# Optimization experiments

Hardware: AMD Instinct MI355X
Metric: run time of the kernel (lower is better)

The kernel has to match this reference:

```python
import jax, jax.numpy as jnp
import numpy as np

N_NODES = 100000
N_EDGES = 1600000
NODE_D = 64
EDGE_D = 48
U_D = 32
N_GRAPHS = 64
HIDDEN = 128
OUT_D = 64
IN_D = NODE_D + EDGE_D + U_D  # 144


def setup_inputs() -> dict:
    key = jax.random.key(0)
    ks = jax.random.split(key, 10)
    x = jax.random.normal(ks[0], (N_NODES, NODE_D), dtype=jnp.float32)
    edge_index = jax.random.randint(ks[1], (2, N_EDGES), 0, N_NODES, dtype=jnp.int64)
    edge_attr = jax.random.normal(ks[2], (N_EDGES, EDGE_D), dtype=jnp.float32)
    u = jax.random.normal(ks[3], (N_GRAPHS, U_D), dtype=jnp.float32)
    batch = jnp.sort(jax.random.randint(ks[4], (N_NODES,), 0, N_GRAPHS, dtype=jnp.int64))
    # FCNN params: Linear(144,128) -> relu -> Linear(128,128) -> relu -> Linear(128,64)
    W1 = jax.random.normal(ks[5], (IN_D, HIDDEN), dtype=jnp.float32) / np.sqrt(IN_D)
    b1 = jnp.zeros((HIDDEN,), dtype=jnp.float32)
    W2 = jax.random.normal(ks[6], (HIDDEN, HIDDEN), dtype=jnp.float32) / np.sqrt(HIDDEN)
    b2 = jnp.zeros((HIDDEN,), dtype=jnp.float32)
    W3 = jax.random.normal(ks[7], (HIDDEN, OUT_D), dtype=jnp.float32) / np.sqrt(HIDDEN)
    b3 = jnp.zeros((OUT_D,), dtype=jnp.float32)
    return {"x": x, "edge_index": edge_index, "edge_attr": edge_attr, "u": u,
            "batch": batch, "W1": W1, "b1": b1, "W2": W2, "b2": b2, "W3": W3, "b3": b3}


def reference(x, edge_index, edge_attr, u, batch, W1, b1, W2, b2, W3, b3):
    n = x.shape[0]
    seg = edge_index[0]  # source node per edge
    # scatter_mean(edge_attr, edge_index[0], dim=0) -> [N, edge_d]
    sums = jax.ops.segment_sum(edge_attr, seg, num_segments=n)
    cnt = jax.ops.segment_sum(jnp.ones((edge_attr.shape[0],), edge_attr.dtype), seg, num_segments=n)
    v_e = sums / jnp.maximum(cnt, 1.0)[:, None]  # mean, 0 for empty segments
    comb = jnp.concatenate([x, v_e, u[batch]], axis=1)  # [N, 144]
    h = jax.nn.relu(comb @ W1 + b1)
    h = jax.nn.relu(h @ W2 + b2)
    return h @ W3 + b3
```

## Files before the change

kernel.cpp:

```cpp
#include <hip/hip_runtime.h>
#include <hip/hip_bf16.h>

#define NN 100000
#define NE 1600000
#define NODE_D 64
#define EDGE_D 48
#define U_D 32
#define IN_D 144
#define HID 128
#define OUT_D 64
#define BM 64
#define S0 152
#define S1 136
#define SCAN_BS 1024
#define SCAN_NB ((NN + SCAN_BS - 1) / SCAN_BS)

typedef __attribute__((ext_vector_type(8))) short bf16x8;
typedef __attribute__((ext_vector_type(4))) float f32x4;

__device__ __forceinline__ short f2bs(float f) {
  union { __hip_bfloat16 h; short s; } v;
  v.h = __float2bfloat16(f);
  return v.s;
}

__device__ __forceinline__ void st4(unsigned short* p, float4 v) {
  unsigned a = (unsigned)(unsigned short)f2bs(v.x) | ((unsigned)(unsigned short)f2bs(v.y) << 16);
  unsigned b = (unsigned)(unsigned short)f2bs(v.z) | ((unsigned)(unsigned short)f2bs(v.w) << 16);
  *reinterpret_cast<uint2*>(p) = make_uint2(a, b);
}

__global__ __launch_bounds__(256) void hist_kernel(const int* __restrict__ src,
                                                   int* __restrict__ hist) {
  int e = blockIdx.x * 256 + threadIdx.x;
  if (e >= NE) return;
  atomicAdd(&hist[src[e]], 1);
}

__global__ __launch_bounds__(256) void bsum_kernel(const int* __restrict__ hist,
                                                   int* __restrict__ bsum) {
  const int b = blockIdx.x, tid = threadIdx.x;
  const int base = b * SCAN_BS + tid * 4;
  int4 v = make_int4(0, 0, 0, 0);
  if (base + 3 < NN) v = *reinterpret_cast<const int4*>(&hist[base]);
  else {
    int t[4] = {0, 0, 0, 0};
    for (int k = 0; k < 4; ++k) if (base + k < NN) t[k] = hist[base + k];
    v = make_int4(t[0], t[1], t[2], t[3]);
  }
  int s = v.x + v.y + v.z + v.w;
  for (int d = 32; d; d >>= 1) s += __shfl_down(s, d, 64);
  __shared__ int ws[4];
  if ((tid & 63) == 0) ws[tid >> 6] = s;
  __syncthreads();
  if (tid == 0) bsum[b] = ws[0] + ws[1] + ws[2] + ws[3];
}

__global__ __launch_bounds__(128) void bscan_kernel(const int* __restrict__ bsum,
                                                    int* __restrict__ bpre) {
  const int t = threadIdx.x;
  const int lane = t & 63, wave = t >> 6;
  int v = (t < SCAN_NB) ? bsum[t] : 0;
  int incl = v;
  for (int d = 1; d < 64; d <<= 1) {
    int q = __shfl_up(incl, d, 64);
    if (lane >= d) incl += q;
  }
  __shared__ int wtot[2];
  if (lane == 63) wtot[wave] = incl;
  __syncthreads();
  int add = (wave == 1) ? wtot[0] : 0;
  if (t < SCAN_NB) bpre[t] = incl - v + add;
}

__global__ __launch_bounds__(256) void offsets_kernel(const int* __restrict__ hist,
                                                      const int* __restrict__ bpre,
                                                      int* __restrict__ offsets,
                                                      int* __restrict__ cursor) {
  const int b = blockIdx.x, tid = threadIdx.x;
  const int base = b * SCAN_BS + tid * 4;
  const int lane = tid & 63, wave = tid >> 6;
  int4 v = make_int4(0, 0, 0, 0);
  if (base + 3 < NN) v = *reinterpret_cast<const int4*>(&hist[base]);
  else {
    int t[4] = {0, 0, 0, 0};
    for (int k = 0; k < 4; ++k) if (base + k < NN) t[k] = hist[base + k];
    v = make_int4(t[0], t[1], t[2], t[3]);
  }
  const int tsum = v.x + v.y + v.z + v.w;
  int incl = tsum;
  for (int d = 1; d < 64; d <<= 1) {
    int q = __shfl_up(incl, d, 64);
    if (lane >= d) incl += q;
  }
  __shared__ int ws[4];
  __shared__ int wpre[4];
  if (lane == 63) ws[wave] = incl;
  __syncthreads();
  if (tid == 0) {
    int r = 0;
    for (int w = 0; w < 4; ++w) { wpre[w] = r; r += ws[w]; }
  }
  __syncthreads();
  int run = bpre[b] + wpre[wave] + incl - tsum;
  int vals[4] = {v.x, v.y, v.z, v.w};
  for (int k = 0; k < 4; ++k) {
    int i = base + k;
    if (i < NN) { offsets[i] = run; cursor[i] = run; run += vals[k]; }
  }
}

__global__ __launch_bounds__(256) void permute_kernel(const int* __restrict__ src,
                                                      int* __restrict__ cursor,
                                                      int* __restrict__ perm) {
  int e = blockIdx.x * 256 + threadIdx.x;
  if (e >= NE) return;
  int s = src[e];
  int pos = atomicAdd(&cursor[s], 1);
  perm[pos] = e;
}

__global__ __launch_bounds__(256) void gather_mean_kernel(
    const float* __restrict__ ea, const int* __restrict__ perm,
    const int* __restrict__ hist, const int* __restrict__ offsets,
    unsigned short* __restrict__ mean) {
  const int node = (blockIdx.x * 256 + threadIdx.x) >> 6;
  const int lane = threadIdx.x & 63;
  if (node >= NN) return;
  const int g = lane >> 4;
  const int c = lane & 15;
  const int deg = hist[node];
  const int off = offsets[node];

  float4 acc = make_float4(0.f, 0.f, 0.f, 0.f);
  if (c < 12) {
    const float* bc = ea + (size_t)c * 4;
    int j = g;
    for (; j + 4 < deg; j += 8) {
      int e0 = perm[off + j];
      int e1 = perm[off + j + 4];
      float4 v0 = *reinterpret_cast<const float4*>(bc + (size_t)e0 * EDGE_D);
      float4 v1 = *reinterpret_cast<const float4*>(bc + (size_t)e1 * EDGE_D);
      acc.x += v0.x + v1.x;
      acc.y += v0.y + v1.y;
      acc.z += v0.z + v1.z;
      acc.w += v0.w + v1.w;
    }
    if (j < deg) {
      int e0 = perm[off + j];
      float4 v0 = *reinterpret_cast<const float4*>(bc + (size_t)e0 * EDGE_D);
      acc.x += v0.x; acc.y += v0.y; acc.z += v0.z; acc.w += v0.w;
    }
  }
#pragma unroll
  for (int d = 32; d >= 16; d >>= 1) {
    acc.x += __shfl_xor(acc.x, d, 64);
    acc.y += __shfl_xor(acc.y, d, 64);
    acc.z += __shfl_xor(acc.z, d, 64);
    acc.w += __shfl_xor(acc.w, d, 64);
  }
  if (lane < 12) {
    float inv = (deg > 0) ? 1.0f / (float)deg : 0.0f;
    st4(&mean[(size_t)node * EDGE_D + lane * 4],
        make_float4(acc.x * inv, acc.y * inv, acc.z * inv, acc.w * inv));
  }
}

__global__ __launch_bounds__(256) void mlp_kernel(
    const float* __restrict__ x, const unsigned short* __restrict__ mean,
    const float* __restrict__ u, const int* __restrict__ batch,
    const float* __restrict__ W1, const float* __restrict__ b1,
    const float* __restrict__ W2, const float* __restrict__ b2,
    const float* __restrict__ W3, const float* __restrict__ b3,
    float* __restrict__ out) {
  __shared__ unsigned short act0[BM][S0];
  __shared__ unsigned short act1[BM][S1];

  const int tid = threadIdx.x;
  const int lane = tid & 63;
  const int wid = tid >> 6;
  const int lr = lane & 15;
  const int lg = lane >> 4;
  const int node0 = blockIdx.x * BM;

  const bf16x8 az = {0, 0, 0, 0, 0, 0, 0, 0};

  for (int i = tid; i < BM * (NODE_D / 4); i += 256) {
    int r = i >> 4, q = i & 15;
    int node = node0 + r;
    float4 v = make_float4(0.f, 0.f, 0.f, 0.f);
    if (node < NN) v = reinterpret_cast<const float4*>(x)[(size_t)node * 16 + q];
    st4(&act0[r][q * 4], v);
  }
  for (int i = tid; i < BM * (EDGE_D / 4); i += 256) {
    int r = i / 12, q = i - r * 12;
    int node = node0 + r;
    uint2 v = make_uint2(0, 0);
    if (node < NN) v = *reinterpret_cast<const uint2*>(&mean[(size_t)node * EDGE_D + q * 4]);
    *reinterpret_cast<uint2*>(&act0[r][NODE_D + q * 4]) = v;
  }
  for (int i = tid; i < BM * (U_D / 4); i += 256) {
    int r = i >> 3, q = i & 7;
    int node = node0 + r;
    float4 v = make_float4(0.f, 0.f, 0.f, 0.f);
    if (node < NN) {
      int b = batch[node];
      v = reinterpret_cast<const float4*>(u)[(size_t)b * 8 + q];
    }
    st4(&act0[r][NODE_D + EDGE_D + q * 4], v);
  }
  __syncthreads();

  {
    const int n0 = wid * 32;
    bf16x8 wf[5][2];
#pragma unroll
    for (int t = 0; t < 5; ++t) {
#pragma unroll
      for (int nf = 0; nf < 2; ++nf) {
        const int kb = t * 32 + lg * 8;
        const int n = n0 + nf * 16 + lr;
        bf16x8 r = az;
#pragma unroll
        for (int j = 0; j < 8; ++j) {
          int k = kb + j;
          if (k < IN_D) r[j] = f2bs(W1[(size_t)k * HID + n]);
        }
        wf[t][nf] = r;
      }
    }
    float bias0 = b1[n0 + lr], bias1 = b1[n0 + 16 + lr];
    f32x4 acc[4][2];
#pragma unroll
    for (int mf = 0; mf < 4; ++mf) {
      acc[mf][0] = (f32x4){bias0, bias0, bias0, bias0};
      acc[mf][1] = (f32x4){bias1, bias1, bias1, bias1};
    }
#pragma unroll
    for (int t = 0; t < 5; ++t) {
#pragma unroll
      for (int mf = 0; mf < 4; ++mf) {
        bf16x8 a;
        if (t < 4) {
          a = *reinterpret_cast<const bf16x8*>(&act0[mf * 16 + lr][t * 32 + lg * 8]);
        } else {
          a = az;
          if (lg < 2)
            a = *reinterpret_cast<const bf16x8*>(&act0[mf * 16 + lr][128 + lg * 8]);
        }
        acc[mf][0] = __builtin_amdgcn_mfma_f32_16x16x32_bf16(a, wf[t][0], acc[mf][0], 0, 0, 0);
        acc[mf][1] = __builtin_amdgcn_mfma_f32_16x16x32_bf16(a, wf[t][1], acc[mf][1], 0, 0, 0);
      }
    }
#pragma unroll
    for (int mf = 0; mf < 4; ++mf)
#pragma unroll
      for (int nf = 0; nf < 2; ++nf)
#pragma unroll
        for (int r = 0; r < 4; ++r)
          act1[mf * 16 + lg * 4 + r][n0 + nf * 16 + lr] =
              (unsigned short)f2bs(fmaxf(acc[mf][nf][r], 0.f));
  }
  __syncthreads();

  {
    const int n0 = wid * 32;
    bf16x8 wf[4][2];
#pragma unroll
    for (int t = 0; t < 4; ++t) {
#pragma unroll
      for (int nf = 0; nf < 2; ++nf) {
        const int kb = t * 32 + lg * 8;
        const int n = n0 + nf * 16 + lr;
        bf16x8 r;
#pragma unroll
        for (int j = 0; j < 8; ++j) r[j] = f2bs(W2[(size_t)(kb + j) * HID + n]);
        wf[t][nf] = r;
      }
    }
    float bias0 = b2[n0 + lr], bias1 = b2[n0 + 16 + lr];
    f32x4 acc[4][2];
#pragma unroll
    for (int mf = 0; mf < 4; ++mf) {
      acc[mf][0] = (f32x4){bias0, bias0, bias0, bias0};
      acc[mf][1] = (f32x4){bias1, bias1, bias1, bias1};
    }
#pragma unroll
    for (int t = 0; t < 4; ++t) {
#pragma unroll
      for (int mf = 0; mf < 4; ++mf) {
        bf16x8 a = *reinterpret_cast<const bf16x8*>(&act1[mf * 16 + lr][t * 32 + lg * 8]);
        acc[mf][0] = __builtin_amdgcn_mfma_f32_16x16x32_bf16(a, wf[t][0], acc[mf][0], 0, 0, 0);
        acc[mf][1] = __builtin_amdgcn_mfma_f32_16x16x32_bf16(a, wf[t][1], acc[mf][1], 0, 0, 0);
      }
    }
    __syncthreads();
#pragma unroll
    for (int mf = 0; mf < 4; ++mf)
#pragma unroll
      for (int nf = 0; nf < 2; ++nf)
#pragma unroll
        for (int r = 0; r < 4; ++r)
          act0[mf * 16 + lg * 4 + r][n0 + nf * 16 + lr] =
              (unsigned short)f2bs(fmaxf(acc[mf][nf][r], 0.f));
  }
  __syncthreads();

  {
    const int n0 = wid * 16;
    bf16x8 wf[4];
#pragma unroll
    for (int t = 0; t < 4; ++t) {
      const int kb = t * 32 + lg * 8;
      const int n = n0 + lr;
      bf16x8 r;
#pragma unroll
      for (int j = 0; j < 8; ++j) r[j] = f2bs(W3[(size_t)(kb + j) * OUT_D + n]);
      wf[t] = r;
    }
    float bias = b3[n0 + lr];
    f32x4 acc[4];
#pragma unroll
    for (int mf = 0; mf < 4; ++mf) acc[mf] = (f32x4){bias, bias, bias, bias};
#pragma unroll
    for (int t = 0; t < 4; ++t) {
#pragma unroll
      for (int mf = 0; mf < 4; ++mf) {
        bf16x8 a = *reinterpret_cast<const bf16x8*>(&act0[mf * 16 + lr][t * 32 + lg * 8]);
        acc[mf] = __builtin_amdgcn_mfma_f32_16x16x32_bf16(a, wf[t], acc[mf], 0, 0, 0);
      }
    }
#pragma unroll
    for (int mf = 0; mf < 4; ++mf)
#pragma unroll
      for (int r = 0; r < 4; ++r) {
        int node = node0 + mf * 16 + lg * 4 + r;
        if (node < NN) out[(size_t)node * OUT_D + n0 + lr] = acc[mf][r];
      }
  }
}

extern "C" void kernel_launch(void* const* d_in, const int* in_sizes, int n_in,
                              void* d_out, int out_size, void* d_ws, size_t ws_size,
                              hipStream_t stream) {
  const float* x   = (const float*)d_in[0];
  const int* ei    = (const int*)d_in[1];
  const float* ea  = (const float*)d_in[2];
  const float* u   = (const float*)d_in[3];
  const int* batch = (const int*)d_in[4];
  const float* W1  = (const float*)d_in[5];
  const float* b1  = (const float*)d_in[6];
  const float* W2  = (const float*)d_in[7];
  const float* b2  = (const float*)d_in[8];
  const float* W3  = (const float*)d_in[9];
  const float* b3  = (const float*)d_in[10];
  float* out = (float*)d_out;

  unsigned short* mean = (unsigned short*)d_ws;
  int* hist    = (int*)(mean + (size_t)NN * EDGE_D);
  int* offsets = hist + NN;
  int* cursor  = offsets + NN;
  int* perm    = cursor + NN;
  int* bsum    = perm + NE;
  int* bpre    = bsum + SCAN_NB;

  hipMemsetAsync(hist, 0, NN * sizeof(int), stream);

  hist_kernel<<<(NE + 255) / 256, 256, 0, stream>>>(ei, hist);
  bsum_kernel<<<SCAN_NB, 256, 0, stream>>>(hist, bsum);
  bscan_kernel<<<1, 128, 0, stream>>>(bsum, bpre);
  offsets_kernel<<<SCAN_NB, 256, 0, stream>>>(hist, bpre, offsets, cursor);
  permute_kernel<<<(NE + 255) / 256, 256, 0, stream>>>(ei, cursor, perm);
  gather_mean_kernel<<<(NN * 64 + 255) / 256, 256, 0, stream>>>(ea, perm, hist, offsets, mean);
  mlp_kernel<<<(NN + BM - 1) / BM, 256, 0, stream>>>(x, mean, u, batch,
                                                     W1, b1, W2, b2, W3, b3, out);
}
```

Measured before the change: 339.7 us.

## Fuse edge-mean gather into MLP kernel and prepack bf16 weights

Moves the per-node edge-attribute mean gather into the MLP kernel, writing the means straight into shared memory instead of round-tripping a bf16 mean buffer through global memory. Weights are converted once to bf16 in a transposed layout by a setup kernel that also zeroes the histogram, replacing hipMemsetAsync and the per-block strided scalar weight conversion. The histogram and permute kernels now handle two edges per thread with int2 loads, and permute uses nontemporal stores. Running the gather inside the MLP blocks lowers gather parallelism per node (16 lanes per node, 4 nodes sequentially per group), which may hurt latency hiding.

```diff
diff --git a/kernel.cpp b/kernel.cpp
--- a/kernel.cpp
+++ b/kernel.cpp
@@ -14,6 +14,11 @@
 #define S1 136
 #define SCAN_BS 1024
 #define SCAN_NB ((NN + SCAN_BS - 1) / SCAN_BS)
+#define W1K 160
+#define NW1 (HID * W1K)
+#define NW2 (HID * HID)
+#define NW3 (OUT_D * HID)
+#define NWTOT (NW1 + NW2 + NW3)
 
 typedef __attribute__((ext_vector_type(8))) short bf16x8;
 typedef __attribute__((ext_vector_type(4))) float f32x4;
@@ -30,11 +35,45 @@
   *reinterpret_cast<uint2*>(p) = make_uint2(a, b);
 }
 
+__global__ __launch_bounds__(256) void setup_kernel(
+    int* __restrict__ hist,
+    const float* __restrict__ W1, const float* __restrict__ W2,
+    const float* __restrict__ W3, unsigned short* __restrict__ Wp) {
+  const int b = blockIdx.x, tid = threadIdx.x;
+  if (b < SCAN_NB) {
+    int base = b * SCAN_BS + tid * 4;
+    if (base + 3 < NN) {
+      *reinterpret_cast<int4*>(&hist[base]) = make_int4(0, 0, 0, 0);
+    } else {
+      for (int k = 0; k < 4; ++k)
+        if (base + k < NN) hist[base + k] = 0;
+    }
+    return;
+  }
+  int gid = (b - SCAN_NB) * 256 + tid;
+  if (gid >= NWTOT) return;
+  float v;
+  if (gid < NW1) {
+    int n = gid / W1K, k = gid - n * W1K;
+    v = (k < IN_D) ? W1[(size_t)k * HID + n] : 0.f;
+  } else if (gid < NW1 + NW2) {
+    int i2 = gid - NW1;
+    int n = i2 >> 7, k = i2 & 127;
+    v = W2[(size_t)k * HID + n];
+  } else {
+    int i3 = gid - NW1 - NW2;
+    int n = i3 >> 7, k = i3 & 127;
+    v = W3[(size_t)k * OUT_D + n];
+  }
+  Wp[gid] = (unsigned short)f2bs(v);
+}
+
 __global__ __launch_bounds__(256) void hist_kernel(const int* __restrict__ src,
                                                    int* __restrict__ hist) {
-  int e = blockIdx.x * 256 + threadIdx.x;
-  if (e >= NE) return;
-  atomicAdd(&hist[src[e]], 1);
+  int i = blockIdx.x * 256 + threadIdx.x;
+  int2 s = *reinterpret_cast<const int2*>(&src[i * 2]);
+  atomicAdd(&hist[s.x], 1);
+  atomicAdd(&hist[s.y], 1);
 }
 
 __global__ __launch_bounds__(256) void bsum_kernel(const int* __restrict__ hist,
@@ -113,66 +152,22 @@
 __global__ __launch_bounds__(256) void permute_kernel(const int* __restrict__ src,
                                                       int* __restrict__ cursor,
                                                       int* __restrict__ perm) {
-  int e = blockIdx.x * 256 + threadIdx.x;
-  if (e >= NE) return;
-  int s = src[e];
-  int pos = atomicAdd(&cursor[s], 1);
-  perm[pos] = e;
-}
-
-__global__ __launch_bounds__(256) void gather_mean_kernel(
-    const float* __restrict__ ea, const int* __restrict__ perm,
-    const int* __restrict__ hist, const int* __restrict__ offsets,
-    unsigned short* __restrict__ mean) {
-  const int node = (blockIdx.x * 256 + threadIdx.x) >> 6;
-  const int lane = threadIdx.x & 63;
-  if (node >= NN) return;
-  const int g = lane >> 4;
-  const int c = lane & 15;
-  const int deg = hist[node];
-  const int off = offsets[node];
-
-  float4 acc = make_float4(0.f, 0.f, 0.f, 0.f);
-  if (c < 12) {
-    const float* bc = ea + (size_t)c * 4;
-    int j = g;
-    for (; j + 4 < deg; j += 8) {
-      int e0 = perm[off + j];
-      int e1 = perm[off + j + 4];
-      float4 v0 = *reinterpret_cast<const float4*>(bc + (size_t)e0 * EDGE_D);
-      float4 v1 = *reinterpret_cast<const float4*>(bc + (size_t)e1 * EDGE_D);
-      acc.x += v0.x + v1.x;
-      acc.y += v0.y + v1.y;
-      acc.z += v0.z + v1.z;
-      acc.w += v0.w + v1.w;
-    }
-    if (j < deg) {
-      int e0 = perm[off + j];
-      float4 v0 = *reinterpret_cast<const float4*>(bc + (size_t)e0 * EDGE_D);
-      acc.x += v0.x; acc.y += v0.y; acc.z += v0.z; acc.w += v0.w;
-    }
-  }
-#pragma unroll
-  for (int d = 32; d >= 16; d >>= 1) {
-    acc.x += __shfl_xor(acc.x, d, 64);
-    acc.y += __shfl_xor(acc.y, d, 64);
-    acc.z += __shfl_xor(acc.z, d, 64);
-    acc.w += __shfl_xor(acc.w, d, 64);
-  }
-  if (lane < 12) {
-    float inv = (deg > 0) ? 1.0f / (float)deg : 0.0f;
-    st4(&mean[(size_t)node * EDGE_D + lane * 4],
-        make_float4(acc.x * inv, acc.y * inv, acc.z * inv, acc.w * inv));
-  }
-}
-
-__global__ __launch_bounds__(256) void mlp_kernel(
-    const float* __restrict__ x, const unsigned short* __restrict__ mean,
+  int i = blockIdx.x * 256 + threadIdx.x;
+  int2 s = *reinterpret_cast<const int2*>(&src[i * 2]);
+  int e0 = i * 2, e1 = i * 2 + 1;
+  int p0 = atomicAdd(&cursor[s.x], 1);
+  __builtin_nontemporal_store(e0, &perm[p0]);
+  int p1 = atomicAdd(&cursor[s.y], 1);
+  __builtin_nontemporal_store(e1, &perm[p1]);
+}
+
+__global__ __launch_bounds__(256) void fused_kernel(
+    const float* __restrict__ x, const float* __restrict__ ea,
     const float* __restrict__ u, const int* __restrict__ batch,
-    const float* __restrict__ W1, const float* __restrict__ b1,
-    const float* __restrict__ W2, const float* __restrict__ b2,
-    const float* __restrict__ W3, const float* __restrict__ b3,
-    float* __restrict__ out) {
+    const int* __restrict__ perm, const int* __restrict__ hist,
+    const int* __restrict__ offsets, const unsigned short* __restrict__ Wp,
+    const float* __restrict__ b1, const float* __restrict__ b2,
+    const float* __restrict__ b3, float* __restrict__ out) {
   __shared__ unsigned short act0[BM][S0];
   __shared__ unsigned short act1[BM][S1];
 
@@ -183,7 +178,58 @@
   const int lg = lane >> 4;
   const int node0 = blockIdx.x * BM;
 
+  const unsigned short* Wp1 = Wp;
+  const unsigned short* Wp2 = Wp + NW1;
+  const unsigned short* Wp3 = Wp + NW1 + NW2;
+
   const bf16x8 az = {0, 0, 0, 0, 0, 0, 0, 0};
+
+  {
+    const int g = tid >> 4;
+    const int c = tid & 15;
+    const int gb = (g & 3) * 16;
+    for (int i = 0; i < 4; ++i) {
+      const int nl = g * 4 + i;
+      const int node = node0 + nl;
+      int deg = 0, off = 0;
+      if (node < NN) { deg = hist[node]; off = offsets[node]; }
+      float4 acc = make_float4(0.f, 0.f, 0.f, 0.f);
+      for (int base = 0; base < deg; base += 16) {
+        int rem = deg - base;
+        int m = rem < 16 ? rem : 16;
+        int pv = 0;
+        if (c < m) pv = perm[off + base + c];
+        int jj = 0;
+        for (; jj + 3 < m; jj += 4) {
+          int e0 = __shfl(pv, gb + jj, 64);
+          int e1 = __shfl(pv, gb + jj + 1, 64);
+          int e2 = __shfl(pv, gb + jj + 2, 64);
+          int e3 = __shfl(pv, gb + jj + 3, 64);
+          if (c < 12) {
+            float4 v0 = *reinterpret_cast<const float4*>(ea + (size_t)e0 * EDGE_D + c * 4);
+            float4 v1 = *reinterpret_cast<const float4*>(ea + (size_t)e1 * EDGE_D + c * 4);
+            float4 v2 = *reinterpret_cast<const float4*>(ea + (size_t)e2 * EDGE_D + c * 4);
+            float4 v3 = *reinterpret_cast<const float4*>(ea + (size_t)e3 * EDGE_D + c * 4);
+            acc.x += (v0.x + v1.x) + (v2.x + v3.x);
+            acc.y += (v0.y + v1.y) + (v2.y + v3.y);
+            acc.z += (v0.z + v1.z) + (v2.z + v3.z);
+            acc.w += (v0.w + v1.w) + (v2.w + v3.w);
+          }
+        }
+        for (; jj < m; ++jj) {
+          int e0 = __shfl(pv, gb + jj, 64);
+          if (c < 12) {
+            float4 v0 = *reinterpret_cast<const float4*>(ea + (size_t)e0 * EDGE_D + c * 4);
+            acc.x += v0.x; acc.y += v0.y; acc.z += v0.z; acc.w += v0.w;
+          }
+        }
+      }
+      float inv = (deg > 0) ? 1.0f / (float)deg : 0.0f;
+      if (c < 12)
+        st4(&act0[nl][NODE_D + c * 4],
+            make_float4(acc.x * inv, acc.y * inv, acc.z * inv, acc.w * inv));
+    }
+  }
 
   for (int i = tid; i < BM * (NODE_D / 4); i += 256) {
     int r = i >> 4, q = i & 15;
@@ -191,13 +237,6 @@
     float4 v = make_float4(0.f, 0.f, 0.f, 0.f);
     if (node < NN) v = reinterpret_cast<const float4*>(x)[(size_t)node * 16 + q];
     st4(&act0[r][q * 4], v);
-  }
-  for (int i = tid; i < BM * (EDGE_D / 4); i += 256) {
-    int r = i / 12, q = i - r * 12;
-    int node = node0 + r;
-    uint2 v = make_uint2(0, 0);
-    if (node < NN) v = *reinterpret_cast<const uint2*>(&mean[(size_t)node * EDGE_D + q * 4]);
-    *reinterpret_cast<uint2*>(&act0[r][NODE_D + q * 4]) = v;
   }
   for (int i = tid; i < BM * (U_D / 4); i += 256) {
     int r = i >> 3, q = i & 7;
@@ -215,20 +254,11 @@
     const int n0 = wid * 32;
     bf16x8 wf[5][2];
 #pragma unroll
-    for (int t = 0; t < 5; ++t) {
-#pragma unroll
-      for (int nf = 0; nf < 2; ++nf) {
-        const int kb = t * 32 + lg * 8;
-        const int n = n0 + nf * 16 + lr;
-        bf16x8 r = az;
-#pragma unroll
-        for (int j = 0; j < 8; ++j) {
-          int k = kb + j;
-          if (k < IN_D) r[j] = f2bs(W1[(size_t)k * HID + n]);
-        }
-        wf[t][nf] = r;
-      }
-    }
+    for (int t = 0; t < 5; ++t)
+#pragma unroll
+      for (int nf = 0; nf < 2; ++nf)
+        wf[t][nf] = *reinterpret_cast<const bf16x8*>(
+            &Wp1[(size_t)(n0 + nf * 16 + lr) * W1K + t * 32 + lg * 8]);
     float bias0 = b1[n0 + lr], bias1 = b1[n0 + 16 + lr];
     f32x4 acc[4][2];
 #pragma unroll
@@ -267,17 +297,11 @@
     const int n0 = wid * 32;
     bf16x8 wf[4][2];
 #pragma unroll
-    for (int t = 0; t < 4; ++t) {
-#pragma unroll
-      for (int nf = 0; nf < 2; ++nf) {
-        const int kb = t * 32 + lg * 8;
-        const int n = n0 + nf * 16 + lr;
-        bf16x8 r;
-#pragma unroll
-        for (int j = 0; j < 8; ++j) r[j] = f2bs(W2[(size_t)(kb + j) * HID + n]);
-        wf[t][nf] = r;
-      }
-    }
+    for (int t = 0; t < 4; ++t)
+#pragma unroll
+      for (int nf = 0; nf < 2; ++nf)
+        wf[t][nf] = *reinterpret_cast<const bf16x8*>(
+            &Wp2[(size_t)(n0 + nf * 16 + lr) * HID + t * 32 + lg * 8]);
     float bias0 = b2[n0 + lr], bias1 = b2[n0 + 16 + lr];
     f32x4 acc[4][2];
 #pragma unroll
@@ -310,14 +334,9 @@
     const int n0 = wid * 16;
     bf16x8 wf[4];
 #pragma unroll
-    for (int t = 0; t < 4; ++t) {
-      const int kb = t * 32 + lg * 8;
-      const int n = n0 + lr;
-      bf16x8 r;
-#pragma unroll
-      for (int j = 0; j < 8; ++j) r[j] = f2bs(W3[(size_t)(kb + j) * OUT_D + n]);
-      wf[t] = r;
-    }
+    for (int t = 0; t < 4; ++t)
+      wf[t] = *reinterpret_cast<const bf16x8*>(
+          &Wp3[(size_t)(n0 + lr) * HID + t * 32 + lg * 8]);
     float bias = b3[n0 + lr];
     f32x4 acc[4];
 #pragma unroll
@@ -356,22 +375,21 @@
   const float* b3  = (const float*)d_in[10];
   float* out = (float*)d_out;
 
-  unsigned short* mean = (unsigned short*)d_ws;
-  int* hist    = (int*)(mean + (size_t)NN * EDGE_D);
+  int* hist    = (int*)d_ws;
   int* offsets = hist + NN;
   int* cursor  = offsets + NN;
   int* perm    = cursor + NN;
   int* bsum    = perm + NE;
   int* bpre    = bsum + SCAN_NB;
-
-  hipMemsetAsync(hist, 0, NN * sizeof(int), stream);
-
-  hist_kernel<<<(NE + 255) / 256, 256, 0, stream>>>(ei, hist);
+  unsigned short* Wp = (unsigned short*)(bpre + SCAN_NB + 60);
+
+  const int wblocks = (NWTOT + 255) / 256;
+  setup_kernel<<<SCAN_NB + wblocks, 256, 0, stream>>>(hist, W1, W2, W3, Wp);
+  hist_kernel<<<NE / 512, 256, 0, stream>>>(ei, hist);
   bsum_kernel<<<SCAN_NB, 256, 0, stream>>>(hist, bsum);
   bscan_kernel<<<1, 128, 0, stream>>>(bsum, bpre);
   offsets_kernel<<<SCAN_NB, 256, 0, stream>>>(hist, bpre, offsets, cursor);
-  permute_kernel<<<(NE + 255) / 256, 256, 0, stream>>>(ei, cursor, perm);
-  gather_mean_kernel<<<(NN * 64 + 255) / 256, 256, 0, stream>>>(ea, perm, hist, offsets, mean);
-  mlp_kernel<<<(NN + BM - 1) / BM, 256, 0, stream>>>(x, mean, u, batch,
-                                                     W1, b1, W2, b2, W3, b3, out);
-}
+  permute_kernel<<<NE / 512, 256, 0, stream>>>(ei, cursor, perm);
+  fused_kernel<<<(NN + BM - 1) / BM, 256, 0, stream>>>(
+      x, ea, u, batch, perm, hist, offsets, Wp, b1, b2, b3, out);
+}
```

Result: faster. 330.5 us (-2.7%).
